# Optimization experiments

Hardware: AMD Instinct MI355X
Metric: run time of the kernel (lower is better)

The kernel has to match this reference:

```python
import jax, jax.numpy as jnp
import numpy as np

DG = 8            # deformable_groups
MAX_RES = 10.0    # max_residual_magnitude
K = 9             # 3x3 kernel positions


def conv3(x, w, b):
    y = jax.lax.conv_general_dilated(x, w, (1, 1), [(1, 1), (1, 1)],
                                     dimension_numbers=('NCHW', 'OIHW', 'NCHW'))
    return y + b[None, :, None, None]


def lrelu(v):
    return jnp.where(v >= 0, v, 0.1 * v)


def deform_conv2d(x, offset, mask, weight, bias):
    # x: [B,C,H,W]; offset: [B,2*DG*K,H,W] (per group, K points, (y,x) interleaved)
    # mask: [B,DG*K,H,W]; weight: [O,C,3,3]; stride=1, pad=1, dil=1, groups=1
    B, C, H, W = x.shape
    Cg = C // DG
    off = offset.reshape(B, DG, K, 2, H, W)
    dtype = x.dtype
    dy = (jnp.arange(K) // 3 - 1).astype(dtype)
    dx = (jnp.arange(K) % 3 - 1).astype(dtype)
    py = off[:, :, :, 0] + jnp.arange(H, dtype=dtype)[None, None, None, :, None] + dy[None, None, :, None, None]
    px = off[:, :, :, 1] + jnp.arange(W, dtype=dtype)[None, None, None, None, :] + dx[None, None, :, None, None]
    y0 = jnp.floor(py)
    x0 = jnp.floor(px)
    x_flat = x.reshape(B, DG, Cg, H * W)
    m = mask.reshape(B, DG, K, H, W)
    acc = jnp.zeros((B, DG, Cg, K, H, W), dtype=dtype)
    for iy, wy in ((y0, y0 + 1.0 - py), (y0 + 1.0, py - y0)):
        for ix, wx in ((x0, x0 + 1.0 - px), (x0 + 1.0, px - x0)):
            valid = (iy >= 0) & (iy < H) & (ix >= 0) & (ix < W)
            yi = jnp.clip(iy, 0, H - 1).astype(jnp.int32)
            xi = jnp.clip(ix, 0, W - 1).astype(jnp.int32)
            idx = (yi * W + xi).reshape(B, DG, 1, K * H * W)
            g = jnp.take_along_axis(x_flat, idx, axis=3).reshape(B, DG, Cg, K, H, W)
            wgt = (wy * wx * valid.astype(dtype) * m)[:, :, None]  # mask folded in
            acc = acc + g * wgt
    O = weight.shape[0]
    out = jnp.einsum('bgckhw,ogck->bohw', acc, weight.reshape(O, DG, Cg, K))
    return out + bias[None, :, None, None]


def setup_inputs() -> dict:
    key = jax.random.key(0)
    ks = jax.random.split(key, 12)
    B, C, H, W = 4, 64, 128, 128
    inp = {
        'x': jax.random.normal(ks[0], (B, C, H, W), jnp.float32),
        'x_warped0': jax.random.normal(ks[1], (B, C, H, W), jnp.float32),
        'x_current': jax.random.normal(ks[2], (B, C, H, W), jnp.float32),
        'flow0': jax.random.normal(ks[3], (B, 2, H, W), jnp.float32),
        'w1': jax.random.normal(ks[4], (64, 130, 3, 3), jnp.float32) * 0.05,
        'b1': jnp.zeros((64,), jnp.float32),
        'w2': jax.random.normal(ks[5], (64, 64, 3, 3), jnp.float32) * 0.05,
        'b2': jnp.zeros((64,), jnp.float32),
        'w3': jax.random.normal(ks[6], (64, 64, 3, 3), jnp.float32) * 0.05,
        'b3': jnp.zeros((64,), jnp.float32),
        'w4': jax.random.normal(ks[7], (216, 64, 3, 3), jnp.float32) * 0.05,
        'b4': jnp.zeros((216,), jnp.float32),
        'weight': jax.random.normal(ks[8], (64, 64, 3, 3), jnp.float32) * 0.05,
        'bias': jnp.zeros((64,), jnp.float32),
    }
    return inp


def reference(x, x_warped0, x_current, flow0, w1, b1, w2, b2, w3, b3, w4, b4, weight, bias):
    # conv_offset stack on cat([x_warped0, x_current, flow0])
    feat = jnp.concatenate([x_warped0, x_current, flow0], axis=1)  # [B, 2C+2, H, W]
    o = lrelu(conv3(feat, w1, b1))
    o = lrelu(conv3(o, w2, b2))
    o = lrelu(conv3(o, w3, b3))
    o = conv3(o, w4, b4)  # [B, 3*K*DG, H, W]
    out1, out2, mask = jnp.split(o, 3, axis=1)
    offset = MAX_RES * jnp.tanh(jnp.concatenate([out1, out2], axis=1))  # [B, 2*K*DG, H, W]
    # flows[0].flip(1).repeat(1, K*DG, 1, 1): (y,x) flow tiled over all sample points
    offset = offset + jnp.tile(flow0[:, ::-1], (1, K * DG, 1, 1))
    mask = jax.nn.sigmoid(mask)
    return deform_conv2d(x, offset, mask, weight, bias)
```

## Files before the change

### kernel.cpp

```cpp
#include <hip/hip_runtime.h>
#include <math.h>

#define HH 128
#define WW 128
#define BB 4
#define HW (HH*WW)

typedef unsigned short u16;
typedef unsigned int u32;
typedef __bf16 bf16x8 __attribute__((ext_vector_type(8)));
typedef float f32x4 __attribute__((ext_vector_type(4)));

__device__ __forceinline__ u16 f2bf(float x) {
    u32 u = __float_as_uint(x);
    return (u16)((u + 0x7fffu + ((u >> 16) & 1u)) >> 16);
}
__device__ __forceinline__ float bf2f(u16 h) {
    return __uint_as_float(((u32)h) << 16);
}
__device__ __forceinline__ bf16x8 ld8(const u16* p) {
    union { uint4 u; bf16x8 v; } c;
    c.u = *(const uint4*)p;
    return c.v;
}
__device__ __forceinline__ bf16x8 cvt8(uint4 u) {
    union { uint4 u; bf16x8 v; } c;
    c.u = u;
    return c.v;
}

__global__ void split_w_k(const float* __restrict__ src, u16* __restrict__ dh,
                          u16* __restrict__ dl, int OC, int OCpad, int CIN, int CINpad)
{
    const int i = blockIdx.x * 256 + threadIdx.x;
    const int tot = OCpad * 9 * CINpad;
    if (i >= tot) return;
    const int oc = i / (9 * CINpad);
    const int r = i - oc * 9 * CINpad;
    const int tap = r / CINpad;
    const int cin = r - tap * CINpad;
    float v = 0.f;
    if (oc < OC && cin < CIN) v = src[((size_t)oc * CIN + cin) * 9 + tap];
    const u16 h = f2bf(v);
    dh[i] = h;
    dl[i] = f2bf(v - bf2f(h));
}

__global__ void pad_bias_k(const float* __restrict__ b, float* __restrict__ bp)
{
    const int i = blockIdx.x * 256 + threadIdx.x;
    if (i < 256) bp[i] = (i < 216) ? b[i] : 0.f;
}

__global__ void pack_dw_k(const float* __restrict__ wt, u16* __restrict__ Apack)
{
    const int i = blockIdx.x * 256 + threadIdx.x;
    if (i >= 36864) return;
    const int jj = i & 7;
    const int fr = (i >> 3) & 15;
    const int m  = (i >> 7) & 3;
    const int fq = (i >> 9) & 3;
    const int kk = i >> 11;
    const int oc = m * 16 + fr;
    const int j  = kk * 32 + fq * 8 + jj;
    const int tap = j >> 3, c = j & 7;
    const int g = tap / 9, kt = tap - g * 9;
    const int ch = g * 8 + c;
    Apack[i] = f2bf(wt[((size_t)oc * 64 + ch) * 9 + kt]);
}

template<int CREC>
__global__ __launch_bounds__(256) void pack_x_k(
    const float* __restrict__ A, const float* __restrict__ B2,
    const float* __restrict__ C3, u16* __restrict__ dst)
{
    const int i = blockIdx.x * 256 + threadIdx.x;
    const int b = i >> 14;
    const int px = i & 16383;
    u16* rec = dst + (size_t)i * (CREC * 2);

#pragma unroll
    for (int g = 0; g < CREC / 32; ++g) {
#pragma unroll
        for (int cb = 0; cb < 4; ++cb) {
            u32 hwv[4], lwv[4];
#pragma unroll
            for (int p = 0; p < 4; ++p) {
                float v[2];
#pragma unroll
                for (int e = 0; e < 2; ++e) {
                    const int c = g * 32 + cb * 8 + p * 2 + e;
                    float vv;
                    if (c < 64)       vv = A[((size_t)(b * 64 + c)) * HW + px];
                    else if (c < 128) vv = B2[((size_t)(b * 64 + c - 64)) * HW + px];
                    else if (c < 130) vv = C3[((size_t)(b * 2 + c - 128)) * HW + px];
                    else              vv = 0.f;
                    v[e] = vv;
                }
                const u16 h0 = f2bf(v[0]), h1 = f2bf(v[1]);
                const u16 l0 = f2bf(v[0] - bf2f(h0)), l1 = f2bf(v[1] - bf2f(h1));
                hwv[p] = (u32)h0 | ((u32)h1 << 16);
                lwv[p] = (u32)l0 | ((u32)l1 << 16);
            }
            uint4 H; H.x = hwv[0]; H.y = hwv[1]; H.z = hwv[2]; H.w = hwv[3];
            uint4 L; L.x = lwv[0]; L.y = lwv[1]; L.z = lwv[2]; L.w = lwv[3];
            *(uint4*)(rec + g * 64 + cb * 16)     = H;
            *(uint4*)(rec + g * 64 + cb * 16 + 8) = L;
        }
    }
}

template<int NCHUNK, int KGLAST, int MODE, bool RELU, bool PACKOUT, int MINW, int NJ>
__global__ __launch_bounds__(256, MINW) void conv_pk_k(
    const u16* __restrict__ Xp, const u16* __restrict__ Wh, const u16* __restrict__ Wl,
    const float* __restrict__ bias, float* __restrict__ outf, u16* __restrict__ outp,
    int OCreal)
{
    const int ROWS = (MODE == 1) ? 8 : 4;
    const int NPX = (ROWS + 2) * 18;
    __shared__ u16 Xs[NPX * 136];
    const int CINpad = (NCHUNK - 1) * 64 + KGLAST * 32;
    const int CRECU16 = CINpad * 2;

    const int tile = blockIdx.x;
    const int h0 = (tile >> 3) * ROWS;
    const int w0 = (tile & 7) * 16;
    const int b = blockIdx.z;
    const int t = threadIdx.x;
    const int lane = t & 63, wv = t >> 6;
    const int fr = lane & 15, fq = lane >> 4;

    const int mg = wv >> 1, rg = wv & 1;
    const int mbase = (MODE == 1) ? (blockIdx.y * 8 + mg * NJ) : 0;

    f32x4 acc0[4];
    f32x4 acc1[NJ][4];
    if (MODE == 0) {
        const float4 bv = *(const float4*)(bias + wv * 16 + 4 * fq);
#pragma unroll
        for (int n = 0; n < 4; ++n) {
            acc0[n][0] = bv.x; acc0[n][1] = bv.y; acc0[n][2] = bv.z; acc0[n][3] = bv.w;
        }
    } else {
#pragma unroll
        for (int m = 0; m < NJ; ++m) {
            const float4 bv = *(const float4*)(bias + (mbase + m) * 16 + 4 * fq);
#pragma unroll
            for (int n = 0; n < 4; ++n) {
                acc1[m][n][0] = bv.x; acc1[m][n][1] = bv.y;
                acc1[m][n][2] = bv.z; acc1[m][n][3] = bv.w;
            }
        }
    }

    const u16* WhL = Wh + (size_t)fr * 9 * CINpad + 8 * fq;
    const u16* WlL = Wl + (size_t)fr * 9 * CINpad + 8 * fq;

#pragma unroll
    for (int chunk = 0; chunk < NCHUNK; ++chunk) {
        const int nkg = (chunk == NCHUNK - 1) ? KGLAST : 2;
        const int nu = nkg * 8;
        __syncthreads();
        for (int s = t; s < NPX * nu; s += 256) {
            const int px = s / nu, o = s - px * nu;
            const int hy = px / 18, hx = px - hy * 18;
            const int gy = h0 + hy - 1, gx = w0 + hx - 1;
            uint4 v; v.x = 0; v.y = 0; v.z = 0; v.w = 0;
            if (gy >= 0 && gy < HH && gx >= 0 && gx < WW)
                v = *(const uint4*)(Xp + ((size_t)(b * HW + gy * WW + gx)) * CRECU16
                                       + chunk * 128 + o * 8);
            *(uint4*)(Xs + px * 136 + o * 8) = v;
        }
        __syncthreads();

        if (MODE == 0) {
#pragma unroll
            for (int tap = 0; tap < 9; ++tap) {
                const int ky = tap / 3, kx = tap % 3;
#pragma unroll
                for (int kg = 0; kg < 2; ++kg) {
                    if (kg >= nkg) break;
                    const size_t off = (size_t)(wv * 144 + tap) * CINpad + chunk * 64 + kg * 32;
                    const bf16x8 Ah = ld8(WhL + off);
                    const bf16x8 Al = ld8(WlL + off);
#pragma unroll
                    for (int n = 0; n < 4; ++n) {
                        const int hp = (n + ky) * 18 + fr + kx;
                        const u16* Bp = Xs + hp * 136 + kg * 64 + fq * 16;
                        const bf16x8 Bh = ld8(Bp);
                        const bf16x8 Bl = ld8(Bp + 8);
                        acc0[n] = __builtin_amdgcn_mfma_f32_16x16x32_bf16(Ah, Bh, acc0[n], 0, 0, 0);
                        acc0[n] = __builtin_amdgcn_mfma_f32_16x16x32_bf16(Ah, Bl, acc0[n], 0, 0, 0);
                        acc0[n] = __builtin_amdgcn_mfma_f32_16x16x32_bf16(Al, Bh, acc0[n], 0, 0, 0);
                    }
                }
            }
        } else {
            auto PF = [&](int tap, bf16x8 (&Dh)[2 * NJ], bf16x8 (&Dl)[2 * NJ]) {
#pragma unroll
                for (int kg = 0; kg < 2; ++kg)
#pragma unroll
                    for (int m = 0; m < NJ; ++m) {
                        const size_t off = (size_t)((mbase + m) * 144 + tap) * CINpad
                                         + chunk * 64 + kg * 32;
                        Dh[kg * NJ + m] = ld8(WhL + off);
                        Dl[kg * NJ + m] = ld8(WlL + off);
                    }
            };
            auto CMP = [&](int tap, bf16x8 (&Dh)[2 * NJ], bf16x8 (&Dl)[2 * NJ]) {
                const int ky = tap / 3, kx = tap - 3 * ky;
#pragma unroll
                for (int kg = 0; kg < 2; ++kg) {
#pragma unroll
                    for (int n = 0; n < 4; ++n) {
                        const int hp = (rg * 4 + n + ky) * 18 + fr + kx;
                        const u16* Bp = Xs + hp * 136 + kg * 64 + fq * 16;
                        const bf16x8 Bh = ld8(Bp);
                        const bf16x8 Bl = ld8(Bp + 8);
#pragma unroll
                        for (int m = 0; m < NJ; ++m) {
                            acc1[m][n] = __builtin_amdgcn_mfma_f32_16x16x32_bf16(Dh[kg * NJ + m], Bh, acc1[m][n], 0, 0, 0);
                            acc1[m][n] = __builtin_amdgcn_mfma_f32_16x16x32_bf16(Dh[kg * NJ + m], Bl, acc1[m][n], 0, 0, 0);
                            acc1[m][n] = __builtin_amdgcn_mfma_f32_16x16x32_bf16(Dl[kg * NJ + m], Bh, acc1[m][n], 0, 0, 0);
                        }
                    }
                }
            };

            bf16x8 PaH[2 * NJ], PaL[2 * NJ], PbH[2 * NJ], PbL[2 * NJ];
            PF(0, PaH, PaL);
#pragma unroll 1
            for (int tp = 0; tp < 4; ++tp) {
                PF(2 * tp + 1, PbH, PbL);
                CMP(2 * tp, PaH, PaL);
                PF(2 * tp + 2, PaH, PaL);
                CMP(2 * tp + 1, PbH, PbL);
            }
            CMP(8, PaH, PaL);
        }
    }

    if (MODE == 1) {
#pragma unroll
        for (int m = 0; m < NJ; ++m) {
            const int mt = mbase + m;
#pragma unroll
            for (int n = 0; n < 4; ++n)
#pragma unroll
                for (int i = 0; i < 4; ++i) {
                    const int oc = mt * 16 + 4 * fq + i;
                    if (oc < OCreal) {
                        float v = acc1[m][n][i];
                        if (mt < 9) {
                            const float a = fabsf(v);
                            const float e = __expf(-2.f * a);
                            float tv = (1.f - e) * __builtin_amdgcn_rcpf(1.f + e);
                            v = 10.f * copysignf(tv, v);
                        } else {
                            v = __builtin_amdgcn_rcpf(1.f + __expf(-v));
                        }
                        outf[((size_t)(b * OCreal + oc)) * HW + (h0 + rg * 4 + n) * WW + w0 + fr] = v;
                    }
                }
        }
    } else if (!PACKOUT) {
#pragma unroll
        for (int n = 0; n < 4; ++n)
#pragma unroll
            for (int i = 0; i < 4; ++i) {
                const int oc = wv * 16 + 4 * fq + i;
                if (oc < OCreal) {
                    float v = acc0[n][i];
                    if (RELU) v = (v >= 0.f) ? v : 0.1f * v;
                    outf[((size_t)(b * OCreal + oc)) * HW + (h0 + n) * WW + w0 + fr] = v;
                }
            }
    } else {
        __syncthreads();
        const int coff = (wv >> 1) * 64 + (((wv << 1) + (fq >> 1)) & 3) * 16 + ((fq & 1) << 2);
#pragma unroll
        for (int n = 0; n < 4; ++n) {
            u16 hh[4], ll[4];
#pragma unroll
            for (int i = 0; i < 4; ++i) {
                float v = acc0[n][i];
                if (RELU) v = (v >= 0.f) ? v : 0.1f * v;
                hh[i] = f2bf(v);
                ll[i] = f2bf(v - bf2f(hh[i]));
            }
            uint2 H, L;
            H.x = (u32)hh[0] | ((u32)hh[1] << 16);
            H.y = (u32)hh[2] | ((u32)hh[3] << 16);
            L.x = (u32)ll[0] | ((u32)ll[1] << 16);
            L.y = (u32)ll[2] | ((u32)ll[3] << 16);
            const int pxe = n * 16 + fr;
            u16* E = Xs + pxe * 136 + coff;
            *(uint2*)E = H;
            *(uint2*)(E + 8) = L;
        }
        __syncthreads();
        for (int i = t; i < 1024; i += 256) {
            const int px = i >> 4, o = i & 15;
            const uint4 v = *(const uint4*)(Xs + px * 136 + o * 8);
            const int gp = (h0 + (px >> 4)) * WW + w0 + (px & 15);
            *(uint4*)(outp + ((size_t)(b * HW + gp)) * 128 + o * 8) = v;
        }
    }
}

__global__ __launch_bounds__(256) void pack_xb_k(
    const float* __restrict__ x, uint4* __restrict__ xqb)
{
    const int i = blockIdx.x * 256 + threadIdx.x;
    const int pix = i & (HW - 1);
    const int g = (i >> 14) & 7;
    const int b = i >> 17;
    const float* xp = x + ((size_t)(b * 64 + g * 8)) * HW + pix;
    u32 w[4];
#pragma unroll
    for (int c2 = 0; c2 < 4; ++c2) {
        const u16 l = f2bf(xp[(size_t)(2 * c2) * HW]);
        const u16 h = f2bf(xp[(size_t)(2 * c2 + 1) * HW]);
        w[c2] = (u32)l | ((u32)h << 16);
    }
    uint4 v; v.x = w[0]; v.y = w[1]; v.z = w[2]; v.w = w[3];
    xqb[(size_t)(b * 8 + g) * HW + pix] = v;
}

__device__ __forceinline__ unsigned pk_bf16(float lo, float hi) {
    unsigned a = __float_as_uint(lo), b = __float_as_uint(hi);
    return ((a + 0x8000u) >> 16) | ((b + 0x8000u) & 0xffff0000u);
}

__global__ __launch_bounds__(512, 8) void deform_fused_k(
    const uint4* __restrict__ xqb, const float* __restrict__ o4,
    const float* __restrict__ flow, const uint4* __restrict__ Apack,
    const float* __restrict__ bias, float* __restrict__ out)
{
    __shared__ u16 sv[32 * 584];

    const int bid0 = blockIdx.x;
    const int bid = (bid0 & 7) * 256 + (bid0 >> 3);
    const int b = bid >> 9;
    const int pix0 = (bid & 511) << 5;
    const int t = threadIdx.x;

    {
        const int gpx = t & 31;
        const int g = (t >> 5) & 7;
        const int kh = t >> 8;
        const int kbase = kh * 4;
        const int pix = pix0 + gpx;
        const int h = pix >> 7, w = pix & (WW - 1);
        const float fy = flow[((size_t)b * 2 + 1) * HW + pix];
        const float fx = flow[((size_t)b * 2 + 0) * HW + pix];
        const float* ob = o4 + (size_t)b * 216 * HW + pix;
        const uint4* qg = xqb + (size_t)(b * 8 + g) * HW;

        int   code[5];
        float w00[5], w01[5], w10[5], w11[5];

#pragma unroll
        for (int j = 0; j < 5; ++j) {
            if (j == 4 && !kh) break;
            const int k = kbase + j;
            const float oy = ob[(size_t)(g * 18 + k * 2) * HW];
            const float ox = ob[(size_t)(g * 18 + k * 2 + 1) * HW];
            const float mm = ob[(size_t)(144 + g * 9 + k) * HW];

            const float ppy = oy + fy + (float)(h + k / 3 - 1);
            const float ppx = ox + fx + (float)(w + k % 3 - 1);

            const float y0f = floorf(ppy), x0f = floorf(ppx);
            const float ly = ppy - y0f, lx = ppx - x0f;
            const int iy0 = (int)y0f, ix0 = (int)x0f;
            const int iy1 = iy0 + 1,  ix1 = ix0 + 1;

            const float vy0 = (iy0 >= 0 && iy0 < HH) ? 1.f : 0.f;
            const float vy1 = (iy1 >= 0 && iy1 < HH) ? 1.f : 0.f;
            const float vx0 = (ix0 >= 0 && ix0 < WW) ? 1.f : 0.f;
            const float vx1 = (ix1 >= 0 && ix1 < WW) ? 1.f : 0.f;

            const int cy0 = min(max(iy0, 0), HH - 1);
            const int cy1 = min(max(iy1, 0), HH - 1);
            const int cx0 = min(max(ix0, 0), WW - 1);
            const int cx1 = min(max(ix1, 0), WW - 1);

            w00[j] = (1.f - ly) * (1.f - lx) * vy0 * vx0 * mm;
            w01[j] = (1.f - ly) * lx         * vy0 * vx1 * mm;
            w10[j] = ly         * (1.f - lx) * vy1 * vx0 * mm;
            w11[j] = ly         * lx         * vy1 * vx1 * mm;

            code[j] = (cy0 * WW + cx0) | ((cx1 - cx0) << 14) | ((cy1 - cy0) << 15);
        }

        u16* svp = sv + gpx * 584 + g * 72 + kbase * 8;
#pragma unroll
        for (int j = 0; j < 5; ++j) {
            if (j == 4 && !kh) break;
            const int i00 = code[j] & 16383;
            const int i01 = i00 + ((code[j] >> 14) & 1);
            const int i10 = i00 + (((code[j] >> 15) & 1) << 7);
            const int i11 = i10 + ((code[j] >> 14) & 1);

            const uint4 A4 = qg[i00];
            const uint4 B4 = qg[i01];
            const uint4 C4 = qg[i10];
            const uint4 D4 = qg[i11];
            const float W00 = w00[j], W01 = w01[j], W10 = w10[j], W11 = w11[j];

            uint4 P;
            u32 pw[4];
#pragma unroll
            for (int c2 = 0; c2 < 4; ++c2) {
                const u32 aw = (&A4.x)[c2], bw = (&B4.x)[c2];
                const u32 cw = (&C4.x)[c2], dw = (&D4.x)[c2];
                const float alo = __uint_as_float(aw << 16), ahi = __uint_as_float(aw & 0xffff0000u);
                const float blo = __uint_as_float(bw << 16), bhi = __uint_as_float(bw & 0xffff0000u);
                const float clo = __uint_as_float(cw << 16), chi = __uint_as_float(cw & 0xffff0000u);
                const float dlo = __uint_as_float(dw << 16), dhi = __uint_as_float(dw & 0xffff0000u);
                const float slo = W00 * alo + W01 * blo + W10 * clo + W11 * dlo;
                const float shi = W00 * ahi + W01 * bhi + W10 * chi + W11 * dhi;
                pw[c2] = pk_bf16(slo, shi);
            }
            P.x = pw[0]; P.y = pw[1]; P.z = pw[2]; P.w = pw[3];
            *(uint4*)(svp + (size_t)j * 8) = P;
        }
    }
    __syncthreads();

    {
        const int lane = t & 63, wv = t >> 6;
        const int mt = wv & 3, nt = wv >> 2;
        const int fr = lane & 15, fq = lane >> 4;

        f32x4 acc;
        acc[0] = 0.f; acc[1] = 0.f; acc[2] = 0.f; acc[3] = 0.f;

#pragma unroll
        for (int kk = 0; kk < 18; ++kk) {
            const bf16x8 A = cvt8(Apack[((kk * 4 + fq) * 4 + mt) * 16 + fr]);
            const bf16x8 Bf = ld8(sv + (size_t)(nt * 16 + fr) * 584 + kk * 32 + fq * 8);
            acc = __builtin_amdgcn_mfma_f32_16x16x32_bf16(A, Bf, acc, 0, 0, 0);
        }

        const float4 bv = *(const float4*)(bias + mt * 16 + 4 * fq);
        const float bb[4] = { bv.x, bv.y, bv.z, bv.w };
        const int pix = pix0 + nt * 16 + fr;
#pragma unroll
        for (int i = 0; i < 4; ++i) {
            const int oc = mt * 16 + 4 * fq + i;
            out[((size_t)b * 64 + oc) * HW + pix] = acc[i] + bb[i];
        }
    }
}

extern "C" void kernel_launch(void* const* d_in, const int* in_sizes, int n_in,
                              void* d_out, int out_size, void* d_ws, size_t ws_size,
                              hipStream_t stream)
{
    const float* x     = (const float*)d_in[0];
    const float* xw    = (const float*)d_in[1];
    const float* xc    = (const float*)d_in[2];
    const float* flow  = (const float*)d_in[3];
    const float* w1    = (const float*)d_in[4];
    const float* b1    = (const float*)d_in[5];
    const float* w2    = (const float*)d_in[6];
    const float* b2    = (const float*)d_in[7];
    const float* w3    = (const float*)d_in[8];
    const float* b3    = (const float*)d_in[9];
    const float* w4    = (const float*)d_in[10];
    const float* b4    = (const float*)d_in[11];
    const float* wt    = (const float*)d_in[12];
    const float* bias  = (const float*)d_in[13];
    float* out = (float*)d_out;

    char* ws = (char*)d_ws;
    u16*   X1p  = (u16*)(ws);
    float* o4   = (float*)(ws);
    u16*   buf1 = (u16*)(ws + 56623104);
    u16*   buf2 = (u16*)(ws + 73400320);
    u16* Apack = (u16*)(ws + 90177536);
    u16* W1h = (u16*)(ws + 90251264);
    u16* W1l = (u16*)(ws + 90435584);
    u16* W2h = (u16*)(ws + 90619904);
    u16* W2l = (u16*)(ws + 90693632);
    u16* W3h = (u16*)(ws + 90767360);
    u16* W3l = (u16*)(ws + 90841088);
    u16* W4h = (u16*)(ws + 90914816);
    u16* W4l = (u16*)(ws + 91209728);
    float* b4p = (float*)(ws + 91504640);

    const dim3 blk(256);

    split_w_k<<<dim3((64 * 9 * 160 + 255) / 256), blk, 0, stream>>>(w1, W1h, W1l, 64, 64, 130, 160);
    split_w_k<<<dim3((64 * 9 * 64 + 255) / 256), blk, 0, stream>>>(w2, W2h, W2l, 64, 64, 64, 64);
    split_w_k<<<dim3((64 * 9 * 64 + 255) / 256), blk, 0, stream>>>(w3, W3h, W3l, 64, 64, 64, 64);
    split_w_k<<<dim3((256 * 9 * 64 + 255) / 256), blk, 0, stream>>>(w4, W4h, W4l, 216, 256, 64, 64);
    pad_bias_k<<<dim3(1), blk, 0, stream>>>(b4, b4p);
    pack_dw_k<<<dim3(144), blk, 0, stream>>>(wt, Apack);

    pack_x_k<160><<<dim3(BB * HW / 256), blk, 0, stream>>>(xw, xc, flow, X1p);
    conv_pk_k<3, 1, 0, true, true, 2, 4><<<dim3(256, 1, BB), blk, 0, stream>>>(
        X1p, W1h, W1l, b1, nullptr, buf1, 64);
    conv_pk_k<1, 2, 0, true, true, 2, 4><<<dim3(256, 1, BB), blk, 0, stream>>>(
        buf1, W2h, W2l, b2, nullptr, buf2, 64);
    conv_pk_k<1, 2, 0, true, true, 2, 4><<<dim3(256, 1, BB), blk, 0, stream>>>(
        buf2, W3h, W3l, b3, nullptr, buf1, 64);
    pack_xb_k<<<dim3(BB * 8 * HW / 256), blk, 0, stream>>>(x, (uint4*)buf2);
    conv_pk_k<1, 2, 1, false, false, 1, 4><<<dim3(128, 2, BB), blk, 0, stream>>>(
        buf1, W4h, W4l, b4p, o4, nullptr, 216);

    deform_fused_k<<<dim3(BB * HW / 32), dim3(512), 0, stream>>>(
        (const uint4*)buf2, o4, flow, (const uint4*)Apack, bias, out);
}
```

Before: 286.8 us.

## Split conv4 input staging by K-group to halve LDS and raise occupancy

The MODE==1 (final offset/mask conv) path now stages the 64-channel input tile in LDS one 32-channel group at a time with a 72-element pixel stride instead of all at once with stride 136. This roughly halves its shared memory footprint. The double-buffered weight prefetch lambdas are replaced by a simple per-tap load, which cuts register pressure. The launch bound for that kernel goes from 1 to 2 waves per SIMD to allow more concurrent blocks, at the cost of an extra barrier pair per block and less latency hiding for the weight loads.

```diff
diff --git a/kernel.cpp b/kernel.cpp
--- a/kernel.cpp
+++ b/kernel.cpp
@@ -117,8 +117,7 @@
     int OCreal)
 {
     const int ROWS = (MODE == 1) ? 8 : 4;
-    const int NPX = (ROWS + 2) * 18;
-    __shared__ u16 Xs[NPX * 136];
+    __shared__ u16 Xs[(MODE == 1) ? (180 * 72) : (108 * 136)];
     const int CINpad = (NCHUNK - 1) * 64 + KGLAST * 32;
     const int CRECU16 = CINpad * 2;
 
@@ -156,24 +155,65 @@
     const u16* WhL = Wh + (size_t)fr * 9 * CINpad + 8 * fq;
     const u16* WlL = Wl + (size_t)fr * 9 * CINpad + 8 * fq;
 
-#pragma unroll
-    for (int chunk = 0; chunk < NCHUNK; ++chunk) {
-        const int nkg = (chunk == NCHUNK - 1) ? KGLAST : 2;
-        const int nu = nkg * 8;
-        __syncthreads();
-        for (int s = t; s < NPX * nu; s += 256) {
-            const int px = s / nu, o = s - px * nu;
-            const int hy = px / 18, hx = px - hy * 18;
-            const int gy = h0 + hy - 1, gx = w0 + hx - 1;
-            uint4 v; v.x = 0; v.y = 0; v.z = 0; v.w = 0;
-            if (gy >= 0 && gy < HH && gx >= 0 && gx < WW)
-                v = *(const uint4*)(Xp + ((size_t)(b * HW + gy * WW + gx)) * CRECU16
-                                       + chunk * 128 + o * 8);
-            *(uint4*)(Xs + px * 136 + o * 8) = v;
-        }
-        __syncthreads();
-
-        if (MODE == 0) {
+    if (MODE == 1) {
+#pragma unroll 1
+        for (int kg = 0; kg < 2; ++kg) {
+            __syncthreads();
+            for (int s = t; s < 180 * 8; s += 256) {
+                const int px = s >> 3, o = s & 7;
+                const int hy = px / 18, hx = px - hy * 18;
+                const int gy = h0 + hy - 1, gx = w0 + hx - 1;
+                uint4 v; v.x = 0; v.y = 0; v.z = 0; v.w = 0;
+                if (gy >= 0 && gy < HH && gx >= 0 && gx < WW)
+                    v = *(const uint4*)(Xp + ((size_t)(b * HW + gy * WW + gx)) * CRECU16
+                                           + kg * 64 + o * 8);
+                *(uint4*)(Xs + px * 72 + o * 8) = v;
+            }
+            __syncthreads();
+
+#pragma unroll
+            for (int tap = 0; tap < 9; ++tap) {
+                const int ky = tap / 3, kx = tap - 3 * ky;
+                bf16x8 Ah[NJ], Al[NJ];
+#pragma unroll
+                for (int m = 0; m < NJ; ++m) {
+                    const size_t off = (size_t)((mbase + m) * 144 + tap) * CINpad + kg * 32;
+                    Ah[m] = ld8(WhL + off);
+                    Al[m] = ld8(WlL + off);
+                }
+#pragma unroll
+                for (int n = 0; n < 4; ++n) {
+                    const int hp = (rg * 4 + n + ky) * 18 + fr + kx;
+                    const u16* Bp = Xs + hp * 72 + fq * 16;
+                    const bf16x8 Bh = ld8(Bp);
+                    const bf16x8 Bl = ld8(Bp + 8);
+#pragma unroll
+                    for (int m = 0; m < NJ; ++m) {
+                        acc1[m][n] = __builtin_amdgcn_mfma_f32_16x16x32_bf16(Ah[m], Bh, acc1[m][n], 0, 0, 0);
+                        acc1[m][n] = __builtin_amdgcn_mfma_f32_16x16x32_bf16(Ah[m], Bl, acc1[m][n], 0, 0, 0);
+                        acc1[m][n] = __builtin_amdgcn_mfma_f32_16x16x32_bf16(Al[m], Bh, acc1[m][n], 0, 0, 0);
+                    }
+                }
+            }
+        }
+    } else {
+#pragma unroll
+        for (int chunk = 0; chunk < NCHUNK; ++chunk) {
+            const int nkg = (chunk == NCHUNK - 1) ? KGLAST : 2;
+            const int nu = nkg * 8;
+            __syncthreads();
+            for (int s = t; s < 108 * nu; s += 256) {
+                const int px = s / nu, o = s - px * nu;
+                const int hy = px / 18, hx = px - hy * 18;
+                const int gy = h0 + hy - 1, gx = w0 + hx - 1;
+                uint4 v; v.x = 0; v.y = 0; v.z = 0; v.w = 0;
+                if (gy >= 0 && gy < HH && gx >= 0 && gx < WW)
+                    v = *(const uint4*)(Xp + ((size_t)(b * HW + gy * WW + gx)) * CRECU16
+                                           + chunk * 128 + o * 8);
+                *(uint4*)(Xs + px * 136 + o * 8) = v;
+            }
+            __syncthreads();
+
 #pragma unroll
             for (int tap = 0; tap < 9; ++tap) {
                 const int ky = tap / 3, kx = tap % 3;
@@ -195,48 +235,6 @@
                     }
                 }
             }
-        } else {
-            auto PF = [&](int tap, bf16x8 (&Dh)[2 * NJ], bf16x8 (&Dl)[2 * NJ]) {
-#pragma unroll
-                for (int kg = 0; kg < 2; ++kg)
-#pragma unroll
-                    for (int m = 0; m < NJ; ++m) {
-                        const size_t off = (size_t)((mbase + m) * 144 + tap) * CINpad
-                                         + chunk * 64 + kg * 32;
-                        Dh[kg * NJ + m] = ld8(WhL + off);
-                        Dl[kg * NJ + m] = ld8(WlL + off);
-                    }
-            };
-            auto CMP = [&](int tap, bf16x8 (&Dh)[2 * NJ], bf16x8 (&Dl)[2 * NJ]) {
-                const int ky = tap / 3, kx = tap - 3 * ky;
-#pragma unroll
-                for (int kg = 0; kg < 2; ++kg) {
-#pragma unroll
-                    for (int n = 0; n < 4; ++n) {
-                        const int hp = (rg * 4 + n + ky) * 18 + fr + kx;
-                        const u16* Bp = Xs + hp * 136 + kg * 64 + fq * 16;
-                        const bf16x8 Bh = ld8(Bp);
-                        const bf16x8 Bl = ld8(Bp + 8);
-#pragma unroll
-                        for (int m = 0; m < NJ; ++m) {
-                            acc1[m][n] = __builtin_amdgcn_mfma_f32_16x16x32_bf16(Dh[kg * NJ + m], Bh, acc1[m][n], 0, 0, 0);
-                            acc1[m][n] = __builtin_amdgcn_mfma_f32_16x16x32_bf16(Dh[kg * NJ + m], Bl, acc1[m][n], 0, 0, 0);
-                            acc1[m][n] = __builtin_amdgcn_mfma_f32_16x16x32_bf16(Dl[kg * NJ + m], Bh, acc1[m][n], 0, 0, 0);
-                        }
-                    }
-                }
-            };
-
-            bf16x8 PaH[2 * NJ], PaL[2 * NJ], PbH[2 * NJ], PbL[2 * NJ];
-            PF(0, PaH, PaL);
-#pragma unroll 1
-            for (int tp = 0; tp < 4; ++tp) {
-                PF(2 * tp + 1, PbH, PbL);
-                CMP(2 * tp, PaH, PaL);
-                PF(2 * tp + 2, PaH, PaL);
-                CMP(2 * tp + 1, PbH, PbL);
-            }
-            CMP(8, PaH, PaL);
         }
     }
 
@@ -508,7 +506,7 @@
     conv_pk_k<1, 2, 0, true, true, 2, 4><<<dim3(256, 1, BB), blk, 0, stream>>>(
         buf2, W3h, W3l, b3, nullptr, buf1, 64);
     pack_xb_k<<<dim3(BB * 8 * HW / 256), blk, 0, stream>>>(x, (uint4*)buf2);
-    conv_pk_k<1, 2, 1, false, false, 1, 4><<<dim3(128, 2, BB), blk, 0, stream>>>(
+    conv_pk_k<1, 2, 1, false, false, 2, 4><<<dim3(128, 2, BB), blk, 0, stream>>>(
         buf1, W4h, W4l, b4p, o4, nullptr, 216);
 
     deform_fused_k<<<dim3(BB * HW / 32), dim3(512), 0, stream>>>(
```

New measurement: 299.3 us. 4.4% more time.
